# Performance work log

Measured on AMD Instinct MI355X. Metric: run time of the kernel, lower is better.

The kernel has to match this reference:

```python
import jax, jax.numpy as jnp
import numpy as np

LAMB = 4.0
TH = -4.0 / LAMB  # threshold from APELoss.__init__
LOSS_WEIGHT = 1.0


def setup_inputs() -> dict:
    key = jax.random.key(0)
    k1, k2 = jax.random.split(key)
    N = 151552  # total anchors
    F = 1024    # foreground anchors (placed first so masks have static shape)
    logits = jax.random.normal(k1, (N,), dtype=jnp.float32)
    targets = jnp.concatenate([jnp.ones((F,), jnp.int32), jnp.zeros((N - F,), jnp.int32)])
    ious = jax.random.uniform(k2, (F,), dtype=jnp.float32)
    return {"logits": logits, "targets": targets, "ious": ious, "num_fg": F}


def reference(logits, targets, ious, num_fg):
    # targets is constructed with all fg (==1) in the first num_fg slots,
    # so logits[targets==1] == logits[:num_fg] (static-shape equivalent).
    fg = logits[:num_fg]          # [F] foreground logits
    bg = logits[num_fg:]          # [B] background logits (targets==0)
    p_min = jnp.min(fg)
    rel_bg = bg >= p_min + TH     # relevant background selection

    # Pairwise fg-vs-bg: [F, B]
    diff_bg = (bg[None, :] - fg[:, None]) * LAMB
    neg_mask = rel_bg[None, :] & (bg[None, :] > fg[:, None] + TH)

    # Pairwise fg-vs-fg: [F, F]
    diff_fg = (fg[None, :] - fg[:, None]) * LAMB
    above = fg[None, :] > fg[:, None] + TH
    pos_mask = (ious[None, :] < ious[:, None]) & above   # lower-IoU fg act as negatives
    tp_mask = (ious[None, :] >= ious[:, None]) & above   # higher/equal-IoU fg are TPs

    # rank = sum sigmoid(FP) + sum sigmoid(TP)  (detached in original)
    fp_sum = (jnp.sum(jax.nn.sigmoid(diff_bg) * neg_mask, axis=1)
              + jnp.sum(jax.nn.sigmoid(diff_fg) * pos_mask, axis=1))
    tp_sum = jnp.sum(jax.nn.sigmoid(diff_fg) * tp_mask, axis=1)
    rank = jax.lax.stop_gradient(fp_sum + tp_sum)

    # BCE(sigmoid(z), 0) = -log(1 - sigmoid(z)) = softplus(z)  (stable form)
    dist = (jnp.sum(jax.nn.softplus(diff_bg) * neg_mask, axis=1)
            + jnp.sum(jax.nn.softplus(diff_fg) * pos_mask, axis=1))

    # Original only appends a loss term when FP_dis is non-empty.
    count = jnp.sum(neg_mask, axis=1) + jnp.sum(pos_mask, axis=1)
    valid = count > 0
    safe_rank = jnp.where(valid, rank, 1.0)
    per = jnp.where(valid, dist * ious / safe_rank, 0.0)
    n_valid = jnp.maximum(jnp.sum(valid), 1)

    return LOSS_WEIGHT * jnp.sum(per) / n_valid.astype(per.dtype) / LAMB
```

## Files before the change

kernel.cpp:

```cpp
#include <hip/hip_runtime.h>
#include <hip/hip_bf16.h>


#define APE_LAMB 4.0f
#define APE_KC   5.770780163555856f
#define APE_LN2  0.6931471805599453f
#define NINF     (-__builtin_inff())

__device__ __forceinline__ float exp2g(float x) { return __builtin_amdgcn_exp2f(x); }
__device__ __forceinline__ float log2g(float x) { return __builtin_amdgcn_logf(x); }
__device__ __forceinline__ float rcpg(float x)  { return __builtin_amdgcn_rcpf(x); }

constexpr int   B_BINS  = 1024;
constexpr int   NB      = 16;
constexpr int   TPB     = 256;
constexpr float BIN_LO  = -5.12f;
constexpr float BIN_DL  = 0.01f;
constexpr float BIN_INV = 100.0f;
constexpr float M1SCALE = 268435456.0f;
constexpr float M1INV   = 3.725290298461914e-09f;
constexpr int   ROWS_E  = 4;
constexpr int   ROWS_B  = 4;

#define ST_AGENT(p, v) __hip_atomic_store((p), (v), __ATOMIC_RELAXED, __HIP_MEMORY_SCOPE_AGENT)
#define LD_AGENT(p)    __hip_atomic_load((p), __ATOMIC_RELAXED, __HIP_MEMORY_SCOPE_AGENT)

__global__ __launch_bounds__(TPB) void ape_phase1(
    const float* __restrict__ logits, const float* __restrict__ ious,
    int F, int M, int chunkH,
    float2* __restrict__ gH, float* __restrict__ bmaxA,
    float* __restrict__ dist2, float* __restrict__ rank2, float* __restrict__ cnt2,
    int* __restrict__ ctr)
{
    const int tid  = threadIdx.x;
    const int lane = tid & 63, wid = tid >> 6;

    if (blockIdx.x == 0 && tid == 0) *ctr = 0;

    if ((int)blockIdx.x < NB) {
        __shared__ int hc[B_BINS];
        __shared__ int hm[B_BINS];
        for (int b = tid; b < B_BINS; b += TPB) { hc[b] = 0; hm[b] = 0; }
        __syncthreads();

        const float* bg = logits + F;
        const int start = (int)blockIdx.x * chunkH;
        const int end   = min(start + chunkH, M);
        float bmax = NINF;

        for (int j = start + tid * 4; j < end; j += TPB * 4) {
            float v[4];
            if (j + 4 <= end) {
                float4 q = *reinterpret_cast<const float4*>(bg + j);
                v[0] = q.x; v[1] = q.y; v[2] = q.z; v[3] = q.w;
            } else {
#pragma unroll
                for (int k = 0; k < 4; ++k) v[k] = (j + k < end) ? bg[j + k] : NINF;
            }
#pragma unroll
            for (int k = 0; k < 4; ++k) {
                if (j + k >= end) continue;
                float x = v[k];
                bmax = fmaxf(bmax, x);
                int b = (int)((x - BIN_LO) * BIN_INV);
                b = min(max(b, 0), B_BINS - 1);
                float c = fmaf((float)b, BIN_DL, BIN_LO + 0.5f * BIN_DL);
                int q = __float2int_rn((x - c) * M1SCALE);
                atomicAdd(&hc[b], 1);
                atomicAdd(&hm[b], q);
            }
        }
        __syncthreads();
        const int base = (int)blockIdx.x * B_BINS;
        for (int b = tid; b < B_BINS; b += TPB)
            gH[base + b] = make_float2((float)hc[b], (float)hm[b] * M1INV);

        __shared__ float rm[4];
        for (int off = 32; off > 0; off >>= 1) bmax = fmaxf(bmax, __shfl_down(bmax, off));
        if (lane == 0) rm[wid] = bmax;
        __syncthreads();
        if (tid == 0)
            bmaxA[blockIdx.x] = fmaxf(fmaxf(rm[0], rm[1]), fmaxf(rm[2], rm[3]));
    } else {
        const int i0 = ((int)blockIdx.x - NB) * ROWS_B;
        float fgl[ROWS_B], ioui[ROWS_B];
#pragma unroll
        for (int r = 0; r < ROWS_B; ++r) {
            int i = i0 + r;
            fgl[r]  = (i < F) ? logits[i] * APE_KC : __builtin_inff();
            ioui[r] = (i < F) ? ious[i] : 0.f;
        }
        float dist[ROWS_B], rank[ROWS_B], cnt[ROWS_B];
#pragma unroll
        for (int r = 0; r < ROWS_B; ++r) { dist[r]=0.f; rank[r]=0.f; cnt[r]=0.f; }

        for (int j = tid; j < F; j += TPB) {
            float fjl  = logits[j] * APE_KC;
            float iouj = ious[j];
#pragma unroll
            for (int r = 0; r < ROWS_B; ++r) {
                float dl = fjl - fgl[r];
                bool above = dl > -APE_KC;
                float dm = above ? dl : NINF;
                float u  = exp2g(dm);
                float o  = 1.0f + u;
                float sig = 1.0f - rcpg(o);
                float spl = log2g(o);
                bool pos = iouj < ioui[r];
                rank[r] += sig;
                dist[r] += pos ? spl : 0.f;
                cnt[r]  += (above && pos) ? 1.f : 0.f;
            }
        }
        __shared__ float redf[4][ROWS_B * 3];
#pragma unroll
        for (int r = 0; r < ROWS_B; ++r) {
            float d = dist[r], a = rank[r], c = cnt[r];
            for (int off = 32; off > 0; off >>= 1) {
                d += __shfl_down(d, off);
                a += __shfl_down(a, off);
                c += __shfl_down(c, off);
            }
            if (lane == 0) { redf[wid][r*3+0]=d; redf[wid][r*3+1]=a; redf[wid][r*3+2]=c; }
        }
        __syncthreads();
        if (tid < ROWS_B * 3) {
            float sum = redf[0][tid] + redf[1][tid] + redf[2][tid] + redf[3][tid];
            int r = tid / 3, q = tid % 3;
            int i = i0 + r;
            if (i < F) {
                if      (q == 0) dist2[i] = sum;
                else if (q == 1) rank2[i] = sum;
                else             cnt2[i]  = sum;
            }
        }
    }
}

__global__ __launch_bounds__(TPB) void ape_phase2(
    const float* __restrict__ logits, const float* __restrict__ ious, int F, int EB,
    const float2* __restrict__ gH, const float* __restrict__ bmaxA,
    const float* __restrict__ dist2, const float* __restrict__ rank2,
    const float* __restrict__ cnt2,
    float* __restrict__ pp, float* __restrict__ pv,
    int* __restrict__ ctr, float* __restrict__ out)
{
    const int tid  = threadIdx.x;
    const int lane = tid & 63, wid = tid >> 6;

    __shared__ float2 h[B_BINS];
    for (int b = tid; b < B_BINS; b += TPB) {
        float c = 0.f, m = 0.f;
#pragma unroll
        for (int s = 0; s < NB; ++s) {
            float2 cm = gH[s * B_BINS + b];
            c += cm.x;
            m += cm.y;
        }
        h[b] = make_float2(c, m);
    }

    const int i0 = (int)blockIdx.x * ROWS_E;
    float fKC[ROWS_E];
#pragma unroll
    for (int r = 0; r < ROWS_E; ++r) {
        int i = i0 + r;
        fKC[r] = (i < F) ? logits[i] * APE_KC : __builtin_inff();
    }
    __syncthreads();

    float rk[ROWS_E], dt[ROWS_E];
#pragma unroll
    for (int r = 0; r < ROWS_E; ++r) { rk[r] = 0.f; dt[r] = 0.f; }

    for (int it = 0; it < B_BINS; it += TPB) {
        const int b = it + tid;
        float2 cm = h[b];
        float cKC  = fmaf((float)b, BIN_DL * APE_KC, (BIN_LO + 0.5f * BIN_DL) * APE_KC);
        float m1x4 = cm.y * APE_LAMB;
        float m1kc = cm.y * APE_KC;
#pragma unroll
        for (int r = 0; r < ROWS_E; ++r) {
            float dl = cKC - fKC[r];
            float dm = (dl > -APE_KC) ? dl : NINF;
            float u  = exp2g(dm);
            float o  = 1.0f + u;
            float rr = rcpg(o);
            float lg = log2g(o);
            float s  = 1.0f - rr;
            rk[r] = fmaf(cm.x, s,  rk[r]);
            rk[r] = fmaf(m1x4, s * rr, rk[r]);
            dt[r] = fmaf(cm.x, lg, dt[r]);
            dt[r] = fmaf(m1kc, s,  dt[r]);
        }
    }

    __shared__ float red[4][ROWS_E * 2];
#pragma unroll
    for (int r = 0; r < ROWS_E; ++r) {
        float a = rk[r], d = dt[r];
        for (int off = 32; off > 0; off >>= 1) {
            a += __shfl_down(a, off);
            d += __shfl_down(d, off);
        }
        if (lane == 0) { red[wid][r*2+0] = a; red[wid][r*2+1] = d; }
    }
    __syncthreads();

    __shared__ int lastFlag;
    if (tid == 0) {
        float gmax = NINF;
#pragma unroll
        for (int k = 0; k < NB; ++k) gmax = fmaxf(gmax, bmaxA[k]);
        float sper = 0.f, sval = 0.f;
#pragma unroll
        for (int r = 0; r < ROWS_E; ++r) {
            int i = i0 + r;
            if (i < F) {
                float rowRank = red[0][r*2+0] + red[1][r*2+0] + red[2][r*2+0] + red[3][r*2+0];
                float rowDist = red[0][r*2+1] + red[1][r*2+1] + red[2][r*2+1] + red[3][r*2+1];
                float rkv = rowRank + rank2[i];
                float dtv = (rowDist + dist2[i]) * APE_LN2;
                bool valid = (gmax > logits[i] - 1.0f) || (cnt2[i] > 0.f);
                if (valid) {
                    sper += dtv * ious[i] / rkv;
                    sval += 1.f;
                }
            }
        }
        ST_AGENT(&pp[blockIdx.x], sper);
        ST_AGENT(&pv[blockIdx.x], sval);
        asm volatile("s_waitcnt vmcnt(0)" ::: "memory");
        int old = __hip_atomic_fetch_add(ctr, 1, __ATOMIC_RELAXED,
                                         __HIP_MEMORY_SCOPE_AGENT);
        lastFlag = (old == EB - 1) ? 1 : 0;
    }
    __syncthreads();
    if (!lastFlag) return;

    float sp = 0.f, sv = 0.f;
    for (int k = tid; k < EB; k += TPB) {
        sp += LD_AGENT(&pp[k]);
        sv += LD_AGENT(&pv[k]);
    }
    __shared__ float rp[4], rv[4];
    for (int off = 32; off > 0; off >>= 1) {
        sp += __shfl_down(sp, off);
        sv += __shfl_down(sv, off);
    }
    if (lane == 0) { rp[wid] = sp; rv[wid] = sv; }
    __syncthreads();
    if (tid == 0) {
        float p = rp[0] + rp[1] + rp[2] + rp[3];
        float v = rv[0] + rv[1] + rv[2] + rv[3];
        out[0] = p / fmaxf(v, 1.f) / APE_LAMB;
    }
}

extern "C" void kernel_launch(void* const* d_in, const int* in_sizes, int n_in,
                              void* d_out, int out_size, void* d_ws, size_t ws_size,
                              hipStream_t stream) {
    const float* logits = (const float*)d_in[0];
    const float* ious   = (const float*)d_in[2];
    const int N = in_sizes[0];
    const int F = in_sizes[2];
    const int M = N - F;

    const int FB = (F + ROWS_B - 1) / ROWS_B;
    const int EB = (F + ROWS_E - 1) / ROWS_E;

    float2* gH   = (float2*)d_ws;
    float* bmaxA = (float*)(gH + NB * B_BINS);
    float* dist2 = bmaxA + NB;
    float* rank2 = dist2 + F;
    float* cnt2  = rank2 + F;
    float* pp    = cnt2 + F;
    float* pv    = pp + EB;
    int*   ctr   = (int*)(pv + EB);

    int chunkH = ((M + NB - 1) / NB + 3) & ~3;
    if (chunkH < 4) chunkH = 4;

    ape_phase1<<<NB + FB, TPB, 0, stream>>>(logits, ious, F, M, chunkH,
                                            gH, bmaxA, dist2, rank2, cnt2, ctr);
    ape_phase2<<<EB, TPB, 0, stream>>>(logits, ious, F, EB, gH, bmaxA,
                                       dist2, rank2, cnt2, pp, pv, ctr,
                                       (float*)d_out);
}
```

Measured before the change: 21.05 us.

## Merge histogram slices via global atomics and per-wave privatized LDS bins

```diff
diff --git a/kernel.cpp b/kernel.cpp
--- a/kernel.cpp
+++ b/kernel.cpp
@@ -12,13 +12,13 @@
 __device__ __forceinline__ float rcpg(float x)  { return __builtin_amdgcn_rcpf(x); }
 
 constexpr int   B_BINS  = 1024;
-constexpr int   NB      = 16;
+constexpr int   NB      = 32;
 constexpr int   TPB     = 256;
 constexpr float BIN_LO  = -5.12f;
 constexpr float BIN_DL  = 0.01f;
 constexpr float BIN_INV = 100.0f;
-constexpr float M1SCALE = 268435456.0f;
-constexpr float M1INV   = 3.725290298461914e-09f;
+constexpr float M1SCALE = 67108864.0f;
+constexpr float M1INV   = 1.4901161193847656e-08f;
 constexpr int   ROWS_E  = 4;
 constexpr int   ROWS_B  = 4;
 
@@ -28,19 +28,19 @@
 __global__ __launch_bounds__(TPB) void ape_phase1(
     const float* __restrict__ logits, const float* __restrict__ ious,
     int F, int M, int chunkH,
-    float2* __restrict__ gH, float* __restrict__ bmaxA,
-    float* __restrict__ dist2, float* __restrict__ rank2, float* __restrict__ cnt2,
-    int* __restrict__ ctr)
+    int* __restrict__ gCnt, int* __restrict__ gM1, float* __restrict__ bmaxA,
+    float* __restrict__ dist2, float* __restrict__ rank2, float* __restrict__ cnt2)
 {
     const int tid  = threadIdx.x;
     const int lane = tid & 63, wid = tid >> 6;
 
-    if (blockIdx.x == 0 && tid == 0) *ctr = 0;
-
     if ((int)blockIdx.x < NB) {
-        __shared__ int hc[B_BINS];
-        __shared__ int hm[B_BINS];
-        for (int b = tid; b < B_BINS; b += TPB) { hc[b] = 0; hm[b] = 0; }
+        __shared__ int hc[4][B_BINS];
+        __shared__ int hm[4][B_BINS];
+        for (int b = tid; b < 4 * B_BINS; b += TPB) {
+            hc[b >> 10][b & (B_BINS - 1)] = 0;
+            hm[b >> 10][b & (B_BINS - 1)] = 0;
+        }
         __syncthreads();
 
         const float* bg = logits + F;
@@ -66,15 +66,19 @@
                 b = min(max(b, 0), B_BINS - 1);
                 float c = fmaf((float)b, BIN_DL, BIN_LO + 0.5f * BIN_DL);
                 int q = __float2int_rn((x - c) * M1SCALE);
-                atomicAdd(&hc[b], 1);
-                atomicAdd(&hm[b], q);
-            }
-        }
-        __syncthreads();
-        const int base = (int)blockIdx.x * B_BINS;
-        for (int b = tid; b < B_BINS; b += TPB)
-            gH[base + b] = make_float2((float)hc[b], (float)hm[b] * M1INV);
-
+                atomicAdd(&hc[wid][b], 1);
+                atomicAdd(&hm[wid][b], q);
+            }
+        }
+        __syncthreads();
+        for (int b = tid; b < B_BINS; b += TPB) {
+            int c = hc[0][b] + hc[1][b] + hc[2][b] + hc[3][b];
+            if (c) {
+                int m = hm[0][b] + hm[1][b] + hm[2][b] + hm[3][b];
+                atomicAdd(&gCnt[b], c);
+                atomicAdd(&gM1[b], m);
+            }
+        }
         __shared__ float rm[4];
         for (int off = 32; off > 0; off >>= 1) bmax = fmaxf(bmax, __shfl_down(bmax, off));
         if (lane == 0) rm[wid] = bmax;
@@ -139,7 +143,8 @@
 
 __global__ __launch_bounds__(TPB) void ape_phase2(
     const float* __restrict__ logits, const float* __restrict__ ious, int F, int EB,
-    const float2* __restrict__ gH, const float* __restrict__ bmaxA,
+    const int* __restrict__ gCnt, const int* __restrict__ gM1,
+    const float* __restrict__ bmaxA,
     const float* __restrict__ dist2, const float* __restrict__ rank2,
     const float* __restrict__ cnt2,
     float* __restrict__ pp, float* __restrict__ pv,
@@ -149,15 +154,14 @@
     const int lane = tid & 63, wid = tid >> 6;
 
     __shared__ float2 h[B_BINS];
-    for (int b = tid; b < B_BINS; b += TPB) {
-        float c = 0.f, m = 0.f;
-#pragma unroll
-        for (int s = 0; s < NB; ++s) {
-            float2 cm = gH[s * B_BINS + b];
-            c += cm.x;
-            m += cm.y;
-        }
-        h[b] = make_float2(c, m);
+    {
+        const int b4 = tid * 4;
+        int4 c4 = *reinterpret_cast<const int4*>(gCnt + b4);
+        int4 m4 = *reinterpret_cast<const int4*>(gM1 + b4);
+        h[b4 + 0] = make_float2((float)c4.x, (float)m4.x * M1INV);
+        h[b4 + 1] = make_float2((float)c4.y, (float)m4.y * M1INV);
+        h[b4 + 2] = make_float2((float)c4.z, (float)m4.z * M1INV);
+        h[b4 + 3] = make_float2((float)c4.w, (float)m4.w * M1INV);
     }
 
     const int i0 = (int)blockIdx.x * ROWS_E;
@@ -269,21 +273,23 @@
     const int FB = (F + ROWS_B - 1) / ROWS_B;
     const int EB = (F + ROWS_E - 1) / ROWS_E;
 
-    float2* gH   = (float2*)d_ws;
-    float* bmaxA = (float*)(gH + NB * B_BINS);
+    int*   gCnt  = (int*)d_ws;
+    int*   gM1   = gCnt + B_BINS;
+    int*   ctr   = gM1 + B_BINS;
+    float* bmaxA = (float*)(ctr + 1);
     float* dist2 = bmaxA + NB;
     float* rank2 = dist2 + F;
     float* cnt2  = rank2 + F;
     float* pp    = cnt2 + F;
     float* pv    = pp + EB;
-    int*   ctr   = (int*)(pv + EB);
 
     int chunkH = ((M + NB - 1) / NB + 3) & ~3;
     if (chunkH < 4) chunkH = 4;
 
+    hipMemsetAsync(gCnt, 0, (2 * B_BINS + 1) * sizeof(int), stream);
     ape_phase1<<<NB + FB, TPB, 0, stream>>>(logits, ious, F, M, chunkH,
-                                            gH, bmaxA, dist2, rank2, cnt2, ctr);
-    ape_phase2<<<EB, TPB, 0, stream>>>(logits, ious, F, EB, gH, bmaxA,
+                                            gCnt, gM1, bmaxA, dist2, rank2, cnt2);
+    ape_phase2<<<EB, TPB, 0, stream>>>(logits, ious, F, EB, gCnt, gM1, bmaxA,
                                        dist2, rank2, cnt2, pp, pv, ctr,
                                        (float*)d_out);
 }
```

After: 24.32 us. 15.5% more time.

## Privatize per-wave LDS histograms and merge partial histograms in separate kernel

Applied to the files above, without the earlier changes.

```diff
diff --git a/kernel.cpp b/kernel.cpp
--- a/kernel.cpp
+++ b/kernel.cpp
@@ -13,6 +13,7 @@
 
 constexpr int   B_BINS  = 1024;
 constexpr int   NB      = 16;
+constexpr int   MB      = 4;
 constexpr int   TPB     = 256;
 constexpr float BIN_LO  = -5.12f;
 constexpr float BIN_DL  = 0.01f;
@@ -38,9 +39,12 @@
     if (blockIdx.x == 0 && tid == 0) *ctr = 0;
 
     if ((int)blockIdx.x < NB) {
-        __shared__ int hc[B_BINS];
-        __shared__ int hm[B_BINS];
-        for (int b = tid; b < B_BINS; b += TPB) { hc[b] = 0; hm[b] = 0; }
+        __shared__ int hc[4][B_BINS];
+        __shared__ int hm[4][B_BINS];
+        for (int b = tid; b < 4 * B_BINS; b += TPB) {
+            hc[b >> 10][b & (B_BINS - 1)] = 0;
+            hm[b >> 10][b & (B_BINS - 1)] = 0;
+        }
         __syncthreads();
 
         const float* bg = logits + F;
@@ -66,15 +70,17 @@
                 b = min(max(b, 0), B_BINS - 1);
                 float c = fmaf((float)b, BIN_DL, BIN_LO + 0.5f * BIN_DL);
                 int q = __float2int_rn((x - c) * M1SCALE);
-                atomicAdd(&hc[b], 1);
-                atomicAdd(&hm[b], q);
+                atomicAdd(&hc[wid][b], 1);
+                atomicAdd(&hm[wid][b], q);
             }
         }
         __syncthreads();
         const int base = (int)blockIdx.x * B_BINS;
-        for (int b = tid; b < B_BINS; b += TPB)
-            gH[base + b] = make_float2((float)hc[b], (float)hm[b] * M1INV);
-
+        for (int b = tid; b < B_BINS; b += TPB) {
+            int c = hc[0][b] + hc[1][b] + hc[2][b] + hc[3][b];
+            int m = hm[0][b] + hm[1][b] + hm[2][b] + hm[3][b];
+            gH[base + b] = make_float2((float)c, (float)m * M1INV);
+        }
         __shared__ float rm[4];
         for (int off = 32; off > 0; off >>= 1) bmax = fmaxf(bmax, __shfl_down(bmax, off));
         if (lane == 0) rm[wid] = bmax;
@@ -137,9 +143,30 @@
     }
 }
 
+__global__ __launch_bounds__(TPB) void ape_merge(
+    const float2* __restrict__ gH, const float* __restrict__ bmaxA,
+    float2* __restrict__ gHm, float* __restrict__ gmaxOut)
+{
+    const int b = (int)blockIdx.x * TPB + threadIdx.x;
+    float c = 0.f, m = 0.f;
+#pragma unroll
+    for (int s = 0; s < NB; ++s) {
+        float2 cm = gH[s * B_BINS + b];
+        c += cm.x;
+        m += cm.y;
+    }
+    gHm[b] = make_float2(c, m);
+    if (blockIdx.x == 0 && threadIdx.x == 0) {
+        float g = NINF;
+#pragma unroll
+        for (int k = 0; k < NB; ++k) g = fmaxf(g, bmaxA[k]);
+        gmaxOut[0] = g;
+    }
+}
+
 __global__ __launch_bounds__(TPB) void ape_phase2(
     const float* __restrict__ logits, const float* __restrict__ ious, int F, int EB,
-    const float2* __restrict__ gH, const float* __restrict__ bmaxA,
+    const float2* __restrict__ gHm, const float* __restrict__ gmaxIn,
     const float* __restrict__ dist2, const float* __restrict__ rank2,
     const float* __restrict__ cnt2,
     float* __restrict__ pp, float* __restrict__ pv,
@@ -149,15 +176,14 @@
     const int lane = tid & 63, wid = tid >> 6;
 
     __shared__ float2 h[B_BINS];
-    for (int b = tid; b < B_BINS; b += TPB) {
-        float c = 0.f, m = 0.f;
-#pragma unroll
-        for (int s = 0; s < NB; ++s) {
-            float2 cm = gH[s * B_BINS + b];
-            c += cm.x;
-            m += cm.y;
-        }
-        h[b] = make_float2(c, m);
+    {
+        const float4* src = reinterpret_cast<const float4*>(gHm);
+        float4 a = src[tid * 2 + 0];
+        float4 b = src[tid * 2 + 1];
+        h[tid * 4 + 0] = make_float2(a.x, a.y);
+        h[tid * 4 + 1] = make_float2(a.z, a.w);
+        h[tid * 4 + 2] = make_float2(b.x, b.y);
+        h[tid * 4 + 3] = make_float2(b.z, b.w);
     }
 
     const int i0 = (int)blockIdx.x * ROWS_E;
@@ -209,9 +235,7 @@
 
     __shared__ int lastFlag;
     if (tid == 0) {
-        float gmax = NINF;
-#pragma unroll
-        for (int k = 0; k < NB; ++k) gmax = fmaxf(gmax, bmaxA[k]);
+        const float gmax = gmaxIn[0];
         float sper = 0.f, sval = 0.f;
 #pragma unroll
         for (int r = 0; r < ROWS_E; ++r) {
@@ -270,20 +294,23 @@
     const int EB = (F + ROWS_E - 1) / ROWS_E;
 
     float2* gH   = (float2*)d_ws;
-    float* bmaxA = (float*)(gH + NB * B_BINS);
-    float* dist2 = bmaxA + NB;
-    float* rank2 = dist2 + F;
-    float* cnt2  = rank2 + F;
-    float* pp    = cnt2 + F;
-    float* pv    = pp + EB;
-    int*   ctr   = (int*)(pv + EB);
+    float2* gHm  = gH + NB * B_BINS;
+    float*  bmaxA = (float*)(gHm + B_BINS);
+    float*  gmax  = bmaxA + NB;
+    float*  dist2 = gmax + 1;
+    float*  rank2 = dist2 + F;
+    float*  cnt2  = rank2 + F;
+    float*  pp    = cnt2 + F;
+    float*  pv    = pp + EB;
+    int*    ctr   = (int*)(pv + EB);
 
     int chunkH = ((M + NB - 1) / NB + 3) & ~3;
     if (chunkH < 4) chunkH = 4;
 
     ape_phase1<<<NB + FB, TPB, 0, stream>>>(logits, ious, F, M, chunkH,
                                             gH, bmaxA, dist2, rank2, cnt2, ctr);
-    ape_phase2<<<EB, TPB, 0, stream>>>(logits, ious, F, EB, gH, bmaxA,
+    ape_merge<<<MB, TPB, 0, stream>>>(gH, bmaxA, gHm, gmax);
+    ape_phase2<<<EB, TPB, 0, stream>>>(logits, ious, F, EB, gHm, gmax,
                                        dist2, rank2, cnt2, pp, pv, ctr,
                                        (float*)d_out);
 }
```

New measurement: 21.45 us. Within noise of the previous version (+1.9%).
